# Optimization experiments

Hardware: AMD Instinct MI355X
Metric: run time of the kernel (lower is better)

Reference implementation:

```python
import jax, jax.numpy as jnp
import numpy as np

B, S, D = 4, 4096, 64

def setup_inputs() -> dict:
    key = jax.random.key(0)
    kq, kk, kv, km = jax.random.split(key, 4)
    q = jax.random.normal(kq, (B, S, D), dtype=jnp.float32)
    k = jax.random.normal(kk, (B, S, D), dtype=jnp.float32)
    v = jax.random.normal(kv, (B, S, D), dtype=jnp.float32)
    # binary keep-mask in {0,1}; log(mask) -> {0, -inf}
    mask = (jax.random.uniform(km, (B, S)) > 0.2).astype(jnp.float32)
    return {"q": q, "k": k, "v": v, "mask": mask}

def reference(q, k, v, mask):
    emb_dim = q.shape[-1]
    qs = q / jnp.asarray(emb_dim, q.dtype) ** 0.5           # [B,S,D] scaled query
    scores = jnp.einsum('bqd,bkd->bqk', qs, k)              # [B,S,S]
    scores = scores + jnp.log(mask)[:, None, :]             # mask keys via log-add
    w = jax.nn.softmax(scores, axis=-1)                     # [B,S,S]
    out = jnp.einsum('bqk,bkd->bqd', w, v)                  # [B,S,D]
    # post-blend: masked query positions pass through the (scaled) query
    return out * mask[..., None] + qs * (1.0 - mask)[..., None]
```

## Files before the change

### kernel.cpp

```cpp
#include <hip/hip_runtime.h>
#include <hip/hip_bf16.h>

#define BATCH 4
#define SEQ   4096
#define DIM   64
#define TK    64
#define LOG2E 1.4426950408889634f

#if __has_builtin(__builtin_amdgcn_mfma_f32_16x16x16bf16_1k)
#define HAVE_1K 1
#else
#define HAVE_1K 0
#endif

#if __has_builtin(__builtin_amdgcn_exp2f)
#define EXP2(x) __builtin_amdgcn_exp2f(x)
#else
#define EXP2(x) exp2f(x)
#endif

typedef __attribute__((ext_vector_type(8))) short bf16x8;
typedef __attribute__((ext_vector_type(4))) short bf16x4;
typedef __attribute__((ext_vector_type(4))) float f32x4;

#define AS1 __attribute__((address_space(1)))
#define AS3 __attribute__((address_space(3)))

static __device__ __forceinline__ short f2bf(float x) {
    __hip_bfloat16 h = __float2bfloat16(x);
    return *reinterpret_cast<short*>(&h);
}
static __device__ __forceinline__ int pk2bf(float lo, float hi) {
    __hip_bfloat162 t = __float22bfloat162_rn(make_float2(lo, hi));
    int r; __builtin_memcpy(&r, &t, 4); return r;
}
static __device__ __forceinline__ bf16x4 mk4(const f32x4& s) {
    int2 t = make_int2(pk2bf(s[0], s[1]), pk2bf(s[2], s[3]));
    bf16x4 r; __builtin_memcpy(&r, &t, 8); return r;
}
static __device__ __forceinline__ f32x4 mfma16(bf16x4 a, bf16x4 b, f32x4 c) {
#if HAVE_1K
    return __builtin_amdgcn_mfma_f32_16x16x16bf16_1k(a, b, c, 0, 0, 0);
#else
    asm("v_mfma_f32_16x16x16_bf16 %0, %1, %2, %0" : "+v"(c) : "v"(a), "v"(b));
    return c;
#endif
}
static __device__ __forceinline__ void async16(const short* g, short* l) {
    __builtin_amdgcn_global_load_lds((const AS1 unsigned int*)g,
                                     (AS3 unsigned int*)l, 16, 0, 0);
}

__global__ __launch_bounds__(256)
void pack_kv(const float* __restrict__ kg, const float* __restrict__ vg,
             const float* __restrict__ mg,
             short* __restrict__ kp, short* __restrict__ vtp)
{
    if (blockIdx.x < 256) {
        #pragma unroll
        for (int i = 0; i < 4; ++i) {
            const int unit = blockIdx.x * 1024 + i * 256 + threadIdx.x;
            const int row = unit >> 4;
            const int d0  = (unit & 15) * 4;
            f32x4 kv = *reinterpret_cast<const f32x4*>(kg + (size_t)row * DIM + d0);
            short4 ks;
            ks.x = f2bf(kv[0]); ks.y = f2bf(kv[1]); ks.z = f2bf(kv[2]); ks.w = f2bf(kv[3]);
            const int gs = (d0 >> 3) ^ (row & 7);
            *reinterpret_cast<short4*>(kp + (size_t)row * DIM + gs * 8 + (d0 & 7)) = ks;
        }
    } else {
        __shared__ float Vl[64][66];
        __shared__ float Ml[64];
        const int tile = blockIdx.x - 256;
        const float* src = vg + (size_t)tile * TK * DIM;
        const int tid = threadIdx.x;
        #pragma unroll
        for (int i = 0; i < 4; ++i) {
            int idx = i * 256 + tid;
            int key = idx >> 4, part = idx & 15;
            f32x4 vv = *reinterpret_cast<const f32x4*>(src + (size_t)key * DIM + part * 4);
            float2* p0 = reinterpret_cast<float2*>(&Vl[key][part * 4]);
            p0[0] = make_float2(vv[0], vv[1]);
            p0[1] = make_float2(vv[2], vv[3]);
        }
        if (tid < 64) Ml[tid] = mg[(size_t)tile * TK + tid];
        __syncthreads();
        #pragma unroll
        for (int i = 0; i < 2; ++i) {
            const int gid = i * 256 + tid;
            const int d = gid >> 3;
            const int G = gid & 7;
            const int qd = G >> 1, u = G & 1;
            alignas(16) short s8[8];
            #pragma unroll
            for (int e = 0; e < 8; ++e) {
                const int v = e >> 2, j = e & 3;
                const int key = (2 * u + v) * 16 + qd * 4 + j;
                s8[e] = f2bf(Vl[key][d] * Ml[key]);
            }
            const int Gs = G ^ (d & 7);
            short* dst = vtp + (size_t)tile * (TK * DIM) + d * TK + Gs * 8;
            *reinterpret_cast<int4*>(dst) = *reinterpret_cast<const int4*>(s8);
        }
    }
}

template<int NSEG>
__global__ __launch_bounds__(256, 4)
void attn_fwd6(const float* __restrict__ qg, const float* __restrict__ mg,
               const short* __restrict__ kp, const short* __restrict__ vtp,
               float* __restrict__ outg, float* __restrict__ part)
{
    constexpr int SEGLEN = SEQ / NSEG;
    constexpr int ITERS  = SEGLEN / TK;

    __shared__ __align__(16) short Kl[2][TK][DIM];
    __shared__ __align__(16) short Vt[2][DIM][TK];

    const int tid  = threadIdx.x;
    const int wave = tid >> 6;
    const int lane = tid & 63;
    const int ln   = lane & 15;
    const int quad = lane >> 4;

    const int qblk = blockIdx.x & 31;
    const int rest = blockIdx.x >> 5;
    const int seg  = (NSEG == 1) ? 0 : (rest & (NSEG - 1));
    const int b    = (NSEG == 1) ? rest : (rest / NSEG);

    const int qw = qblk * 128 + wave * 32;
    const size_t bbase = (size_t)b * SEQ * DIM;

    const short* kb  = kp  + bbase + (size_t)seg * SEGLEN * DIM;
    const short* vb  = vtp + bbase + (size_t)seg * SEGLEN * DIM;
    const float* mgb = mg + (size_t)b * SEQ;

    const int gs0 = quad ^ (ln & 7);

    bf16x8 aq[2][2];
    #pragma unroll
    for (int qt = 0; qt < 2; ++qt) {
        const float* qrow = qg + bbase + (size_t)(qw + qt * 16 + ln) * DIM;
        #pragma unroll
        for (int h = 0; h < 2; ++h) {
            alignas(16) short tmp[8];
            #pragma unroll
            for (int j = 0; j < 8; ++j)
                tmp[j] = f2bf(qrow[quad * 8 + h * 32 + j] * (0.125f * LOG2E));
            aq[qt][h] = *reinterpret_cast<bf16x8*>(tmp);
        }
    }

    f32x4 O[2][4];
    float lacc[2] = {0.f, 0.f};
    #pragma unroll
    for (int qt = 0; qt < 2; ++qt)
        #pragma unroll
        for (int i = 0; i < 4; ++i) O[qt][i] = (f32x4){0.f, 0.f, 0.f, 0.f};

    #pragma unroll
    for (int i = 0; i < 2; ++i) {
        const int c = wave * 2 + i;
        async16(kb + c * 512 + lane * 8, &Kl[0][0][0] + c * 512);
        async16(vb + c * 512 + lane * 8, &Vt[0][0][0] + c * 512);
    }

    for (int t = 0; t < ITERS; ++t) {
        const int buf = t & 1;
        asm volatile("s_waitcnt vmcnt(0)" ::: "memory");
        __syncthreads();

        if (t + 1 < ITERS) {
            const short* gk = kb + (size_t)(t + 1) * TK * DIM;
            const short* gv = vb + (size_t)(t + 1) * TK * DIM;
            #pragma unroll
            for (int i = 0; i < 2; ++i) {
                const int c = wave * 2 + i;
                async16(gk + c * 512 + lane * 8, &Kl[buf ^ 1][0][0] + c * 512);
                async16(gv + c * 512 + lane * 8, &Vt[buf ^ 1][0][0] + c * 512);
            }
        }

        const int key0 = seg * SEGLEN + t * TK;
        const short* klb = &Kl[buf][0][0];
        const short* vtb = &Vt[buf][0][0];

        #pragma unroll
        for (int u = 0; u < 2; ++u) {
            f32x4 m4[2];
            #pragma unroll
            for (int v = 0; v < 2; ++v)
                m4[v] = *reinterpret_cast<const f32x4*>(
                    mgb + key0 + (2 * u + v) * 16 + quad * 4);

            f32x4 sf[2][2];
            #pragma unroll
            for (int v = 0; v < 2; ++v) {
                const int s = 2 * u + v;
                bf16x8 ka0 = *reinterpret_cast<const bf16x8*>(
                    klb + (s * 16 + ln) * DIM + gs0 * 8);
                bf16x8 ka1 = *reinterpret_cast<const bf16x8*>(
                    klb + (s * 16 + ln) * DIM + (gs0 ^ 4) * 8);
                #pragma unroll
                for (int qt = 0; qt < 2; ++qt) {
                    f32x4 acc = (f32x4){0.f, 0.f, 0.f, 0.f};
                    acc = __builtin_amdgcn_mfma_f32_16x16x32_bf16(ka0, aq[qt][0], acc, 0, 0, 0);
                    acc = __builtin_amdgcn_mfma_f32_16x16x32_bf16(ka1, aq[qt][1], acc, 0, 0, 0);
                    sf[qt][v] = acc;
                }
            }

            bf16x4 bp[2][2];
            #pragma unroll
            for (int qt = 0; qt < 2; ++qt) {
                #pragma unroll
                for (int v = 0; v < 2; ++v) {
                    #pragma unroll
                    for (int r = 0; r < 4; ++r) {
                        sf[qt][v][r] = EXP2(sf[qt][v][r]);
                        lacc[qt] = fmaf(sf[qt][v][r], m4[v][r], lacc[qt]);
                    }
                    bp[qt][v] = mk4(sf[qt][v]);
                }
            }

            const int gvu = (quad * 2 + u) ^ (ln & 7);
            #pragma unroll
            for (int ds = 0; ds < 4; ++ds) {
                bf16x8 vf = *reinterpret_cast<const bf16x8*>(
                    vtb + (ds * 16 + ln) * TK + gvu * 8);
                bf16x4 va0 = __builtin_shufflevector(vf, vf, 0, 1, 2, 3);
                bf16x4 va1 = __builtin_shufflevector(vf, vf, 4, 5, 6, 7);
                #pragma unroll
                for (int qt = 0; qt < 2; ++qt) {
                    O[qt][ds] = mfma16(va0, bp[qt][0], O[qt][ds]);
                    O[qt][ds] = mfma16(va1, bp[qt][1], O[qt][ds]);
                }
            }
        }
    }

    #pragma unroll
    for (int qt = 0; qt < 2; ++qt) {
        lacc[qt] += __shfl_xor(lacc[qt], 16);
        lacc[qt] += __shfl_xor(lacc[qt], 32);
    }

    if (NSEG == 1) {
        #pragma unroll
        for (int qt = 0; qt < 2; ++qt) {
            const int qrow_i = qw + qt * 16 + ln;
            const float qm = mgb[qrow_i];
            const float inv = 1.0f / lacc[qt];
            const float* qrow = qg + bbase + (size_t)qrow_i * DIM;
            float* orow = outg + bbase + (size_t)qrow_i * DIM;
            #pragma unroll
            for (int ds = 0; ds < 4; ++ds) {
                const int d0 = ds * 16 + quad * 4;
                f32x4 o4;
                #pragma unroll
                for (int r = 0; r < 4; ++r) o4[r] = O[qt][ds][r] * inv;
                if (qm == 0.0f) {
                    f32x4 q4 = *reinterpret_cast<const f32x4*>(qrow + d0);
                    #pragma unroll
                    for (int r = 0; r < 4; ++r) o4[r] = q4[r] * 0.125f;
                }
                *reinterpret_cast<f32x4*>(orow + d0) = o4;
            }
        }
    } else {
        #pragma unroll
        for (int qt = 0; qt < 2; ++qt) {
            float* pb = part + (size_t)((b * SEQ + qw + qt * 16 + ln) * NSEG + seg) * 68;
            #pragma unroll
            for (int ds = 0; ds < 4; ++ds)
                *reinterpret_cast<f32x4*>(pb + ds * 16 + quad * 4) = O[qt][ds];
            if (quad == 0) pb[64] = lacc[qt];
        }
    }
}

template<int NSEG>
__global__ __launch_bounds__(256)
void combine_p(const float* __restrict__ part, const float* __restrict__ qg,
               const float* __restrict__ mg, float* __restrict__ outg)
{
    const int t = blockIdx.x * 256 + threadIdx.x;
    const int q = t >> 6;
    const int d = t & 63;
    const float* pb = part + (size_t)q * NSEG * 68;
    float acc = 0.f, den = 0.f;
    #pragma unroll
    for (int s = 0; s < NSEG; ++s) {
        acc += pb[s * 68 + d];
        den += pb[s * 68 + 64];
    }
    float out = acc / den;
    if (mg[q] == 0.0f) out = qg[t] * 0.125f;
    outg[t] = out;
}

extern "C" void kernel_launch(void* const* d_in, const int* in_sizes, int n_in,
                              void* d_out, int out_size, void* d_ws, size_t ws_size,
                              hipStream_t stream) {
    (void)in_sizes; (void)n_in; (void)out_size;
    const float* q = (const float*)d_in[0];
    const float* k = (const float*)d_in[1];
    const float* v = (const float*)d_in[2];
    const float* m = (const float*)d_in[3];
    float* out = (float*)d_out;

    const size_t nelem  = (size_t)BATCH * SEQ * DIM;
    const size_t packsz = nelem * 2 * sizeof(short);
    const size_t part8  = (size_t)BATCH * SEQ * 8 * 68 * sizeof(float);
    const size_t part4  = (size_t)BATCH * SEQ * 4 * 68 * sizeof(float);

    short* kp  = (short*)d_ws;
    short* vtp = kp + nelem;
    float* part = (float*)((char*)d_ws + packsz);

    pack_kv<<<dim3(512), dim3(256), 0, stream>>>(k, v, m, kp, vtp);

    if (ws_size >= packsz + part8) {
        attn_fwd6<8><<<dim3(BATCH * 32 * 8), dim3(256), 0, stream>>>(q, m, kp, vtp, out, part);
        combine_p<8><<<dim3(BATCH * SEQ * DIM / 256), dim3(256), 0, stream>>>(part, q, m, out);
    } else if (ws_size >= packsz + part4) {
        attn_fwd6<4><<<dim3(BATCH * 32 * 4), dim3(256), 0, stream>>>(q, m, kp, vtp, out, part);
        combine_p<4><<<dim3(BATCH * SEQ * DIM / 256), dim3(256), 0, stream>>>(part, q, m, out);
    } else {
        attn_fwd6<1><<<dim3(BATCH * 32), dim3(256), 0, stream>>>(q, m, kp, vtp, out, nullptr);
    }
}
```

Measured before the change: 108.0 us.

## Fuse split-KV combine into attention kernel via last-block atomic counter

Removes the separate combine kernel. Each segment block writes its partial output, now stored as bf16, plus its row denominators. It then increments a per-query-block atomic counter, and the last-arriving block reduces all segments and writes the final output. This saves a kernel launch and halves partial-output traffic. In exchange it adds a memset, threadfences and a serialized tail reduction in one block per query tile, and rounds partials to bf16.

```diff
diff --git a/kernel.cpp b/kernel.cpp
--- a/kernel.cpp
+++ b/kernel.cpp
@@ -5,6 +5,7 @@
 #define SEQ   4096
 #define DIM   64
 #define TK    64
+#define TOTQ  (BATCH * SEQ)
 #define LOG2E 1.4426950408889634f
 
 #if __has_builtin(__builtin_amdgcn_mfma_f32_16x16x16bf16_1k)
@@ -29,6 +30,10 @@
 static __device__ __forceinline__ short f2bf(float x) {
     __hip_bfloat16 h = __float2bfloat16(x);
     return *reinterpret_cast<short*>(&h);
+}
+static __device__ __forceinline__ float bf2f(short s) {
+    unsigned int u = ((unsigned int)(unsigned short)s) << 16;
+    float f; __builtin_memcpy(&f, &u, 4); return f;
 }
 static __device__ __forceinline__ int pk2bf(float lo, float hi) {
     __hip_bfloat162 t = __float22bfloat162_rn(make_float2(lo, hi));
@@ -107,15 +112,18 @@
 
 template<int NSEG>
 __global__ __launch_bounds__(256, 4)
-void attn_fwd6(const float* __restrict__ qg, const float* __restrict__ mg,
+void attn_fwd7(const float* __restrict__ qg, const float* __restrict__ mg,
                const short* __restrict__ kp, const short* __restrict__ vtp,
-               float* __restrict__ outg, float* __restrict__ part)
+               float* __restrict__ outg,
+               short* __restrict__ Opart, float* __restrict__ lpart,
+               int* __restrict__ cnt)
 {
     constexpr int SEGLEN = SEQ / NSEG;
     constexpr int ITERS  = SEGLEN / TK;
 
     __shared__ __align__(16) short Kl[2][TK][DIM];
     __shared__ __align__(16) short Vt[2][DIM][TK];
+    __shared__ int sOld;
 
     const int tid  = threadIdx.x;
     const int wave = tid >> 6;
@@ -268,36 +276,56 @@
                 *reinterpret_cast<f32x4*>(orow + d0) = o4;
             }
         }
-    } else {
-        #pragma unroll
-        for (int qt = 0; qt < 2; ++qt) {
-            float* pb = part + (size_t)((b * SEQ + qw + qt * 16 + ln) * NSEG + seg) * 68;
-            #pragma unroll
-            for (int ds = 0; ds < 4; ++ds)
-                *reinterpret_cast<f32x4*>(pb + ds * 16 + quad * 4) = O[qt][ds];
-            if (quad == 0) pb[64] = lacc[qt];
-        }
-    }
-}
-
-template<int NSEG>
-__global__ __launch_bounds__(256)
-void combine_p(const float* __restrict__ part, const float* __restrict__ qg,
-               const float* __restrict__ mg, float* __restrict__ outg)
-{
-    const int t = blockIdx.x * 256 + threadIdx.x;
-    const int q = t >> 6;
-    const int d = t & 63;
-    const float* pb = part + (size_t)q * NSEG * 68;
-    float acc = 0.f, den = 0.f;
-    #pragma unroll
-    for (int s = 0; s < NSEG; ++s) {
-        acc += pb[s * 68 + d];
-        den += pb[s * 68 + 64];
-    }
-    float out = acc / den;
-    if (mg[q] == 0.0f) out = qg[t] * 0.125f;
-    outg[t] = out;
+        return;
+    }
+
+    #pragma unroll
+    for (int qt = 0; qt < 2; ++qt) {
+        const int gq = b * SEQ + qw + qt * 16 + ln;
+        short* ob = Opart + ((size_t)seg * TOTQ + gq) * 64;
+        #pragma unroll
+        for (int ds = 0; ds < 4; ++ds) {
+            bf16x4 o4 = mk4(O[qt][ds]);
+            *reinterpret_cast<bf16x4*>(ob + ds * 16 + quad * 4) = o4;
+        }
+        if (quad == 0) lpart[(size_t)seg * TOTQ + gq] = lacc[qt];
+    }
+
+    __syncthreads();
+    if (tid == 0) {
+        __threadfence();
+        sOld = atomicAdd(cnt + (b * 32 + qblk), 1);
+    }
+    __syncthreads();
+    if (sOld != NSEG - 1) return;
+
+    __threadfence();
+    const int qbase = b * SEQ + qblk * 128;
+    #pragma unroll
+    for (int it = 0; it < 8; ++it) {
+        const int idx = it * 256 + tid;
+        const int qo  = idx >> 4;
+        const int d0  = (idx & 15) * 4;
+        const int gq  = qbase + qo;
+        float a0 = 0.f, a1 = 0.f, a2 = 0.f, a3 = 0.f, den = 0.f;
+        #pragma unroll
+        for (int s = 0; s < NSEG; ++s) {
+            const short* ob = Opart + ((size_t)s * TOTQ + gq) * 64 + d0;
+            short4 o4 = *reinterpret_cast<const short4*>(ob);
+            a0 += bf2f(o4.x); a1 += bf2f(o4.y);
+            a2 += bf2f(o4.z); a3 += bf2f(o4.w);
+            den += lpart[(size_t)s * TOTQ + gq];
+        }
+        const float inv = 1.0f / den;
+        f32x4 o;
+        o[0] = a0 * inv; o[1] = a1 * inv; o[2] = a2 * inv; o[3] = a3 * inv;
+        if (mg[gq] == 0.0f) {
+            f32x4 q4 = *reinterpret_cast<const f32x4*>(qg + (size_t)gq * DIM + d0);
+            #pragma unroll
+            for (int r = 0; r < 4; ++r) o[r] = q4[r] * 0.125f;
+        }
+        *reinterpret_cast<f32x4*>(outg + (size_t)gq * DIM + d0) = o;
+    }
 }
 
 extern "C" void kernel_launch(void* const* d_in, const int* in_sizes, int n_in,
@@ -312,22 +340,24 @@
 
     const size_t nelem  = (size_t)BATCH * SEQ * DIM;
     const size_t packsz = nelem * 2 * sizeof(short);
-    const size_t part8  = (size_t)BATCH * SEQ * 8 * 68 * sizeof(float);
-    const size_t part4  = (size_t)BATCH * SEQ * 4 * 68 * sizeof(float);
-
-    short* kp  = (short*)d_ws;
-    short* vtp = kp + nelem;
-    float* part = (float*)((char*)d_ws + packsz);
-
-    pack_kv<<<dim3(512), dim3(256), 0, stream>>>(k, v, m, kp, vtp);
-
-    if (ws_size >= packsz + part8) {
-        attn_fwd6<8><<<dim3(BATCH * 32 * 8), dim3(256), 0, stream>>>(q, m, kp, vtp, out, part);
-        combine_p<8><<<dim3(BATCH * SEQ * DIM / 256), dim3(256), 0, stream>>>(part, q, m, out);
-    } else if (ws_size >= packsz + part4) {
-        attn_fwd6<4><<<dim3(BATCH * 32 * 4), dim3(256), 0, stream>>>(q, m, kp, vtp, out, part);
-        combine_p<4><<<dim3(BATCH * SEQ * DIM / 256), dim3(256), 0, stream>>>(part, q, m, out);
+    const size_t osz    = (size_t)8 * TOTQ * 64 * sizeof(short);
+    const size_t lsz    = (size_t)8 * TOTQ * sizeof(float);
+    const size_t csz    = 512;
+
+    short* kp   = (short*)d_ws;
+    short* vtp  = kp + nelem;
+    short* Op   = (short*)((char*)d_ws + packsz);
+    float* lp   = (float*)((char*)d_ws + packsz + osz);
+    int*   cnt  = (int*)  ((char*)d_ws + packsz + osz + lsz);
+
+    if (ws_size >= packsz + osz + lsz + csz) {
+        hipMemsetAsync(cnt, 0, csz, stream);
+        pack_kv<<<dim3(512), dim3(256), 0, stream>>>(k, v, m, kp, vtp);
+        attn_fwd7<8><<<dim3(BATCH * 32 * 8), dim3(256), 0, stream>>>(
+            q, m, kp, vtp, out, Op, lp, cnt);
     } else {
-        attn_fwd6<1><<<dim3(BATCH * 32), dim3(256), 0, stream>>>(q, m, kp, vtp, out, nullptr);
-    }
-}
+        pack_kv<<<dim3(512), dim3(256), 0, stream>>>(k, v, m, kp, vtp);
+        attn_fwd7<1><<<dim3(BATCH * 32), dim3(256), 0, stream>>>(
+            q, m, kp, vtp, out, nullptr, nullptr, nullptr);
+    }
+}
```

Result: slower. 165.5 us (+53.3%).
